# Kernel tuning notes

Measured on AMD Instinct MI355X. Metric: run time of the kernel, lower is better.

## Reference

```python
import jax, jax.numpy as jnp
import numpy as np

C = 1.0          # curvature of PoincareBall
SQRT_C = 1.0
MIN_NORM = 1e-15
PROJ_EPS = 4e-3  # float32 boundary eps used by PoincareBall.proj
N_NODES = 50000


def _norm(x):
    return jnp.clip(jnp.linalg.norm(x, axis=-1, keepdims=True), MIN_NORM)


def _artanh(x):
    return jnp.arctanh(jnp.clip(x, -1.0 + 1e-7, 1.0 - 1e-7))


def proj(x):
    # clip points to the open ball of radius (1-eps)/sqrt(c)
    norm = _norm(x)
    maxnorm = (1.0 - PROJ_EPS) / SQRT_C
    return jnp.where(norm > maxnorm, x / norm * maxnorm, x)


def expmap0(u):
    u_norm = _norm(u)
    return jnp.tanh(SQRT_C * u_norm) * u / (SQRT_C * u_norm)


def logmap0(p):
    p_norm = _norm(p)
    return _artanh(SQRT_C * p_norm) * p / (SQRT_C * p_norm)


def mobius_add(x, y):
    x2 = jnp.sum(x * x, -1, keepdims=True)
    y2 = jnp.sum(y * y, -1, keepdims=True)
    xy = jnp.sum(x * y, -1, keepdims=True)
    num = (1.0 + 2.0 * C * xy + C * y2) * x + (1.0 - C * x2) * y
    den = 1.0 + 2.0 * C * xy + C * C * x2 * y2
    return num / jnp.clip(den, MIN_NORM)


def mobius_matvec(m, x):
    x_norm = _norm(x)
    mx = x @ m.T  # [N, d_out]
    mx_norm = _norm(mx)
    res = jnp.tanh(mx_norm / x_norm * _artanh(SQRT_C * x_norm)) * mx / (mx_norm * SQRT_C)
    zero_row = jnp.all(mx == 0, axis=-1, keepdims=True)
    return jnp.where(zero_row, jnp.zeros_like(res), res)


def setup_inputs() -> dict:
    key = jax.random.key(0)
    k = jax.random.split(key, 6)
    n, d_in, d_out, n_edges = N_NODES, 256, 96, 800000
    # points on the Poincare ball
    x = proj(0.02 * jax.random.normal(k[0], (n, d_in), jnp.float32))
    weight = jax.random.normal(k[1], (d_out, d_in), jnp.float32) * (1.0 / np.sqrt(d_in)).astype(np.float32)
    bias = jax.random.normal(k[2], (d_out,), jnp.float32) * 0.01
    edge_row = jax.random.randint(k[3], (n_edges,), 0, n)
    edge_col = jax.random.randint(k[4], (n_edges,), 0, n)
    # normalized adjacency weights ~ 1/avg_degree
    edge_weight = jax.random.uniform(k[5], (n_edges,), jnp.float32) * (1.0 / 16.0)
    return {"x": x, "weight": weight, "bias": bias, "edge_weight": edge_weight,
            "edge_row": edge_row, "edge_col": edge_col}


def reference(x, weight, bias, edge_weight, edge_row, edge_col):
    # --- HypLinear (dropout inactive in eval) ---
    h = proj(mobius_matvec(weight, x))
    hyp_bias = proj(expmap0(bias[None, :]))  # proj_tan0 is identity on the ball
    h = proj(mobius_add(h, hyp_bias))
    # --- HypAgg: spmm(adj, logmap0(h)) then expmap0 ---
    xt = logmap0(h)                                  # [N, d_out]
    msgs = edge_weight[:, None] * xt[edge_col]       # [E, d_out]
    support = jax.ops.segment_sum(msgs, edge_row, num_segments=N_NODES)
    h = proj(expmap0(support))
    # --- HypAct: relu in tangent space, map back (c_in == c_out) ---
    h = proj(expmap0(jax.nn.relu(logmap0(h))))
    return h
```

## Files before the change

### kernel.cpp

```cpp
#include <hip/hip_runtime.h>


typedef __attribute__((ext_vector_type(8))) short short8;
typedef __attribute__((ext_vector_type(4))) float floatx4;

#define DIN 256
#define DOUT 96
#define MAXN 0.996f
#define EPS15 1e-15f
#define ATC (1.0f - 1e-7f)
#define NBK 391
#define CAP 2560
#define TILE 6144

__device__ __forceinline__ float us2f(unsigned short u) {
    unsigned int v = ((unsigned int)u) << 16;
    return __uint_as_float(v);
}
__device__ __forceinline__ unsigned short f2us(float f) {
    unsigned int b = __float_as_uint(f);
    unsigned int r = (b + 0x7FFFu + ((b >> 16) & 1u)) >> 16;
    return (unsigned short)r;
}

__global__ void initzero_kernel(const unsigned short* __restrict__ xraw,
                                const void* __restrict__ bias,
                                const void* __restrict__ wgt,
                                float* __restrict__ ws,
                                int* __restrict__ gcur) {
    int i = blockIdx.x * blockDim.x + threadIdx.x;
    int stride = gridDim.x * blockDim.x;
    for (int k = i; k < NBK * 16; k += stride) gcur[k] = 0;

    if (blockIdx.x == 0 && threadIdx.x < 64) {
        int l = threadIdx.x;
        float v0 = us2f(xraw[l]);
        float v1 = us2f(xraw[64 + l]);
        int big = (!(fabsf(v0) < 1e4f)) || (!(fabsf(v1) < 1e4f));
        #pragma unroll
        for (int m = 32; m >= 1; m >>= 1) big |= __shfl_xor(big, m, 64);
        bool isb = !big;
        if (l == 0) ws[97] = isb ? 1.0f : 0.0f;

        float b0 = isb ? us2f(((const unsigned short*)bias)[l])
                       : ((const float*)bias)[l];
        float b1 = 0.0f;
        if (l < 32)
            b1 = isb ? us2f(((const unsigned short*)bias)[64 + l])
                     : ((const float*)bias)[64 + l];
        float n2 = b0 * b0 + b1 * b1;
        #pragma unroll
        for (int m = 32; m >= 1; m >>= 1) n2 += __shfl_xor(n2, m, 64);
        float bn = fmaxf(sqrtf(n2), EPS15);
        float ef = tanhf(bn) / bn;
        float hn = ef * sqrtf(n2);
        float s = (hn > MAXN) ? MAXN / fmaxf(hn, EPS15) : 1.0f;
        ws[l] = s * ef * b0;
        if (l < 32) ws[64 + l] = s * ef * b1;
        if (l == 0) { float v = s * hn; ws[96] = v * v; }
    }

    if (blockIdx.x >= 1 && blockIdx.x <= 12) {
        int t = threadIdx.x, lane = t & 63;
        float v0 = us2f(xraw[lane]);
        float v1 = us2f(xraw[64 + lane]);
        int big = (!(fabsf(v0) < 1e4f)) || (!(fabsf(v1) < 1e4f));
        #pragma unroll
        for (int m = 32; m >= 1; m >>= 1) big |= __shfl_xor(big, m, 64);
        bool isb = !big;
        uint4* wz = (uint4*)(ws + 128);
        int g = t + 256 * (int)(blockIdx.x - 1);
        int c = g >> 5, j = g & 31;
        int f = c >> 4, mr = c & 15;
        int kt = j >> 2, q = j & 3;
        if (isb) {
            const uint4* wg = (const uint4*)wgt;
            wz[(f * 8 + kt) * 64 + q * 16 + mr] = wg[g];
        } else {
            const float* wgf = (const float*)wgt;
            const float* src = wgf + (size_t)c * DIN + j * 8;
            unsigned short tmp[8];
            #pragma unroll
            for (int z = 0; z < 8; z++) tmp[z] = f2us(src[z]);
            wz[(f * 8 + kt) * 64 + q * 16 + mr] = *(const uint4*)tmp;
        }
    }
}

__global__ void __launch_bounds__(256) part_kernel(
        const void* __restrict__ ew,
        const int* __restrict__ erow,
        const int* __restrict__ ecol,
        const float* __restrict__ ws,
        int* __restrict__ gcur,
        uint2* __restrict__ arena, int E) {
    __shared__ uint2 stage[TILE];
    __shared__ int h[NBK], excl[NBK], cur[NBK], gb[NBK];
    __shared__ int cb[64];

    const int t = threadIdx.x;
    const bool isb = ws[97] != 0.0f;
    const int tb = blockIdx.x * TILE;
    const int tcnt = min(TILE, E - tb);

    for (int i = t; i < NBK; i += 256) h[i] = 0;
    __syncthreads();

    int rw[24]; unsigned int pk[24];
    #pragma unroll
    for (int k = 0; k < 24; k++) {
        int e = tb + t + 256 * k;
        if (e < E) {
            int r = erow[e];
            unsigned int wb = isb ? (unsigned int)((const unsigned short*)ew)[e]
                                  : (unsigned int)f2us(((const float*)ew)[e]);
            rw[k] = r;
            pk[k] = (wb << 16) | (unsigned int)ecol[e];
            atomicAdd(&h[r >> 7], 1);
        } else rw[k] = -1;
    }
    __syncthreads();

    if (t < 64) {
        int s = 0;
        #pragma unroll
        for (int j = 0; j < 8; j++) {
            int b2 = t * 8 + j;
            if (b2 < NBK) s += h[b2];
        }
        int sc = s;
        #pragma unroll
        for (int d = 1; d < 64; d <<= 1) {
            int tt = __shfl_up(sc, d, 64);
            if (t >= d) sc += tt;
        }
        cb[t] = sc - s;
    }
    __syncthreads();
    for (int b2 = t; b2 < NBK; b2 += 256) {
        int base = cb[b2 >> 3];
        int x = 0;
        for (int j = (b2 & ~7); j < b2; j++) x += h[j];
        excl[b2] = base + x;
        cur[b2]  = base + x;
        gb[b2] = atomicAdd(&gcur[b2 * 16], h[b2]);
    }
    __syncthreads();

    #pragma unroll
    for (int k = 0; k < 24; k++) {
        if (rw[k] >= 0) {
            int b2 = rw[k] >> 7;
            int slot = atomicAdd(&cur[b2], 1);
            stage[slot] = make_uint2(pk[k], (unsigned int)rw[k]);
        }
    }
    __syncthreads();

    for (int s = t; s < tcnt; s += 256) {
        uint2 ent = stage[s];
        int b2 = (int)ent.y >> 7;
        int p = gb[b2] + (s - excl[b2]);
        if (p < CAP) arena[(size_t)b2 * CAP + p] = ent;
    }
}

__global__ void __launch_bounds__(256) hypsort_kernel(
        const void* __restrict__ x,
        float* __restrict__ ws,
        unsigned short* __restrict__ xtb,
        const int* __restrict__ gcur,
        uint2* __restrict__ arena,
        uint2* __restrict__ roff,
        int N) {
    __shared__ int h[128], excl[128], cur[128];

    const int t = threadIdx.x;
    const bool isb = ws[97] != 0.0f;
    const int b = blockIdx.x;
    const int rem = b % 3;
    const int b3 = b / 3;

    if (rem == 2) {
        const int idx = b3;
        int cnt = gcur[idx * 16]; if (cnt > CAP) cnt = CAP;
        const size_t ab = (size_t)idx * CAP;

        for (int i = t; i < 128; i += 256) h[i] = 0;
        __syncthreads();

        uint2 ent[10];
        #pragma unroll
        for (int k = 0; k < 10; k++) {
            int j = t + 256 * k;
            if (j < cnt) {
                ent[k] = arena[ab + j];
                atomicAdd(&h[ent[k].y & 127u], 1);
            } else ent[k] = make_uint2(0u, 0u);
        }
        __syncthreads();

        if (t < 64) {
            int a0 = h[2 * t], a1 = h[2 * t + 1];
            int ps = a0 + a1;
            int sc = ps;
            #pragma unroll
            for (int d = 1; d < 64; d <<= 1) {
                int tt = __shfl_up(sc, d, 64);
                if (t >= d) sc += tt;
            }
            int ex = sc - ps;
            excl[2 * t] = ex;      excl[2 * t + 1] = ex + a0;
            cur[2 * t]  = ex;      cur[2 * t + 1]  = ex + a0;
        }
        __syncthreads();

        if (t < 128)
            roff[idx * 128 + t] =
                make_uint2((unsigned int)(ab + excl[t]), (unsigned int)h[t]);
        #pragma unroll
        for (int k = 0; k < 10; k++) {
            int j = t + 256 * k;
            if (j < cnt) {
                int slot = atomicAdd(&cur[ent[k].y & 127u], 1);
                arena[ab + slot] = ent[k];
            }
        }
        return;
    }

    const int idx = b3 * 2 + rem;
    const int lane = t & 63;
    const int wv = t >> 6;
    const int mrow = lane & 15;
    const int quad = lane >> 4;
    const uint4* __restrict__ Wg = (const uint4*)(ws + 128);

    const int r0 = (idx * 4 + wv) * 16;
    if (r0 >= N) return;

    float hbl[6];
    #pragma unroll
    for (int f = 0; f < 6; f++) hbl[f] = ws[mrow + 16 * f];
    const float hb2 = ws[96];

    int xr = r0 + mrow; if (xr >= N) xr = N - 1;
    short8 afrag[8];
    if (isb) {
        const unsigned short* xrow = (const unsigned short*)x + (size_t)xr * DIN + quad * 8;
        #pragma unroll
        for (int kt = 0; kt < 8; kt++)
            afrag[kt] = *(const short8*)(xrow + kt * 32);
    } else {
        const float* xrow = (const float*)x + (size_t)xr * DIN + quad * 8;
        #pragma unroll
        for (int kt = 0; kt < 8; kt++) {
            short8 a;
            #pragma unroll
            for (int j = 0; j < 8; j++) a[j] = (short)f2us(xrow[kt * 32 + j]);
            afrag[kt] = a;
        }
    }

    float xn2p = 0.f;
    #pragma unroll
    for (int kt = 0; kt < 8; kt++)
        #pragma unroll
        for (int j = 0; j < 8; j++) {
            float v = us2f((unsigned short)afrag[kt][j]);
            xn2p = fmaf(v, v, xn2p);
        }
    xn2p += __shfl_xor(xn2p, 16, 64);
    xn2p += __shfl_xor(xn2p, 32, 64);

    floatx4 acc[6];
    #pragma unroll
    for (int f = 0; f < 6; f++) acc[f] = (floatx4){0.f, 0.f, 0.f, 0.f};
    #pragma unroll
    for (int f = 0; f < 6; f++) {
        uint4 bw[8];
        #pragma unroll
        for (int kt = 0; kt < 8; kt++)
            bw[kt] = Wg[(f * 8 + kt) * 64 + lane];
        #pragma unroll
        for (int kt = 0; kt < 8; kt++) {
            short8 bfr = *(const short8*)&bw[kt];
            acc[f] = __builtin_amdgcn_mfma_f32_16x16x32_bf16(afrag[kt], bfr, acc[f], 0, 0, 0);
        }
    }

    float mxn2[4], dmh[4];
    #pragma unroll
    for (int reg = 0; reg < 4; reg++) {
        float a2 = 0.f, ad = 0.f;
        #pragma unroll
        for (int f = 0; f < 6; f++) {
            float v = acc[f][reg];
            a2 = fmaf(v, v, a2);
            ad = fmaf(v, hbl[f], ad);
        }
        mxn2[reg] = a2; dmh[reg] = ad;
    }
    #pragma unroll
    for (int m = 8; m >= 1; m >>= 1)
        #pragma unroll
        for (int reg = 0; reg < 4; reg++) {
            mxn2[reg] += __shfl_xor(mxn2[reg], m, 64);
            dmh[reg]  += __shfl_xor(dmh[reg],  m, 64);
        }

    int sel = mrow & 3;
    float xn2  = __shfl(xn2p, quad * 4 + sel, 64);
    float wmx2 = mxn2[sel], wdmh = dmh[sel];

    float xn  = fmaxf(sqrtf(xn2), EPS15);
    float mxn = fmaxf(sqrtf(wmx2), EPS15);
    float g   = (mxn / xn) * atanhf(fminf(xn, ATC));
    float tg  = tanhf(g);
    float rs0 = tg / mxn;
    float rn  = rs0 * sqrtf(wmx2);
    float s1  = (rn > MAXN) ? MAXN / fmaxf(rn, EPS15) : 1.0f;
    float al  = s1 * rs0;
    float x2  = al * al * wmx2;
    float xy  = al * wdmh;
    float cA  = 1.0f + 2.0f * xy + hb2;
    float cB  = 1.0f - x2;
    float den = fmaxf(1.0f + 2.0f * xy + x2 * hb2, EPS15);
    float p   = cA * al / den;
    float qq  = cB / den;
    float o2  = p*p*wmx2 + 2.0f*p*qq*wdmh + qq*qq*hb2;
    float on  = sqrtf(fmaxf(o2, 0.0f));
    float s2  = (on > MAXN) ? MAXN / fmaxf(on, EPS15) : 1.0f;
    float pn  = fmaxf(s2 * on, EPS15);
    float F   = (atanhf(fminf(pn, ATC)) / pn) * s2;
    float Fp_m = F * p, Fq_m = F * qq;

    float Fp[4], Fq[4];
    #pragma unroll
    for (int reg = 0; reg < 4; reg++) {
        Fp[reg] = __shfl(Fp_m, quad * 16 + reg, 64);
        Fq[reg] = __shfl(Fq_m, quad * 16 + reg, 64);
    }

    #pragma unroll
    for (int reg = 0; reg < 4; reg++) {
        int row = r0 + quad * 4 + reg;
        if (row < N) {
            size_t base = (size_t)row * DOUT + mrow;
            #pragma unroll
            for (int f = 0; f < 6; f++)
                xtb[base + 16 * f] = f2us(fmaf(Fp[reg], acc[f][reg], Fq[reg] * hbl[f]));
        }
    }
}

__global__ void __launch_bounds__(256) rowagg_kernel(
        const unsigned short* __restrict__ xtb,
        const uint2* __restrict__ arena,
        const uint2* __restrict__ roff,
        const float* __restrict__ ws,
        void* __restrict__ out, int N) {
    int wv = threadIdx.x >> 6, lane = threadIdx.x & 63;
    int node = blockIdx.x * 4 + wv;
    if (node >= N) return;
    const bool isb = ws[97] != 0.0f;
    const bool act = lane < 48;

    uint2 ro = roff[node];
    unsigned int start = ro.x;
    int cnt = (int)ro.y;

    float acc0 = 0.f, acc1 = 0.f;

    unsigned int uA[8], uB[8];
    float wA[8], wB[8];

#define ISSUE(BU, BW, B)                                                       \
    _Pragma("unroll")                                                          \
    for (int k = 0; k < 8; k++) {                                              \
        int idx = (B) * 8 + k;                                                 \
        unsigned int ex = (unsigned int)__shfl((int)myx, idx, 64);             \
        BW[k] = __uint_as_float(ex & 0xFFFF0000u);                             \
        const unsigned int* sp =                                               \
            (const unsigned int*)(xtb + (size_t)(ex & 0xFFFFu) * DOUT);        \
        BU[k] = (act && idx < navail) ? sp[lane] : 0u;                         \
    }

#define CONSUME(BU, BW)                                                        \
    _Pragma("unroll")                                                          \
    for (int k = 0; k < 8; k++) {                                              \
        acc0 = fmaf(BW[k], __uint_as_float(BU[k] << 16), acc0);                \
        acc1 = fmaf(BW[k], __uint_as_float(BU[k] & 0xFFFF0000u), acc1);        \
    }

    for (int cs = 0; cs < cnt; cs += 64) {
        int navail = cnt - cs; if (navail > 64) navail = 64;
        unsigned int myx = (lane < navail) ? arena[start + cs + lane].x : 0u;
        int nb = (navail + 7) >> 3;
        ISSUE(uA, wA, 0);
        for (int bb = 1; bb < nb; bb++) {
            if (bb & 1) { ISSUE(uB, wB, bb); CONSUME(uA, wA); }
            else        { ISSUE(uA, wA, bb); CONSUME(uB, wB); }
        }
        if (nb & 1) { CONSUME(uA, wA); }
        else        { CONSUME(uB, wB); }
    }
#undef ISSUE
#undef CONSUME

    float u0 = acc0, u1 = acc1;
    float n2 = u0*u0 + u1*u1;
    #pragma unroll
    for (int m = 32; m >= 1; m >>= 1) n2 += __shfl_xor(n2, m, 64);
    float un = fmaxf(sqrtf(n2), EPS15);
    float ef = tanhf(un) / un;
    float p0 = ef * u0, p1 = ef * u1;
    float pnrm = ef * sqrtf(n2);
    float sc = (pnrm > MAXN) ? MAXN / fmaxf(pnrm, EPS15) : 1.0f;
    p0 *= sc; p1 *= sc; pnrm *= sc;
    float pncl = fmaxf(pnrm, EPS15);
    float lf = atanhf(fminf(pncl, ATC)) / pncl;
    float t0 = fmaxf(lf * p0, 0.0f), t1 = fmaxf(lf * p1, 0.0f);
    float tn2 = t0*t0 + t1*t1;
    #pragma unroll
    for (int m = 32; m >= 1; m >>= 1) tn2 += __shfl_xor(tn2, m, 64);
    float tn = fmaxf(sqrtf(tn2), EPS15);
    float ef2 = tanhf(tn) / tn;
    float en = ef2 * sqrtf(tn2);
    float s2 = (en > MAXN) ? MAXN / fmaxf(en, EPS15) : 1.0f;
    float scale = s2 * ef2;
    float v0 = scale * t0, v1 = scale * t1;

    if (act) {
        if (isb) {
            unsigned int pk = ((unsigned int)f2us(v1) << 16) | (unsigned int)f2us(v0);
            ((unsigned int*)((unsigned short*)out + (size_t)node * DOUT))[lane] = pk;
        } else {
            float2 fv; fv.x = v0; fv.y = v1;
            ((float2*)((float*)out + (size_t)node * DOUT))[lane] = fv;
        }
    }
}

extern "C" void kernel_launch(void* const* d_in, const int* in_sizes, int n_in,
                              void* d_out, int out_size, void* d_ws, size_t ws_size,
                              hipStream_t stream) {
    const void* x    = d_in[0];
    const void* wgt  = d_in[1];
    const void* bias = d_in[2];
    const void* ew   = d_in[3];
    const int* erow  = (const int*)d_in[4];
    const int* ecol  = (const int*)d_in[5];

    int N = out_size / DOUT;
    int E = in_sizes[4];

    float* wsf = (float*)d_ws;
    int* gcur = (int*)(wsf + 128 + 12288);
    uint2* arena = (uint2*)((char*)d_ws + 74688);
    unsigned short* xtb = (unsigned short*)((char*)d_ws + 74688 + (size_t)NBK * CAP * 8);
    uint2* roff = (uint2*)(xtb + (size_t)N * DOUT);

    int Pb = (E + TILE - 1) / TILE;

    initzero_kernel<<<13, 256, 0, stream>>>((const unsigned short*)x, bias, wgt, wsf, gcur);
    part_kernel<<<Pb, 256, 0, stream>>>(ew, erow, ecol, wsf, gcur, arena, E);
    hypsort_kernel<<<3 * NBK, 256, 0, stream>>>(x, wsf, xtb, gcur, arena, roff, N);
    rowagg_kernel<<<(N + 3) / 4, 256, 0, stream>>>(xtb, arena, roff, wsf, d_out, N);
}
```

Measured before the change: 184.8 us.

## Split fused hyp/sort kernel, pad per-row edge lists to multiples of eight

Splits the combined matvec and bucket-sort kernel into separate hyp and sort kernels. The sort stage now pads each row's edge list to a multiple of 8 with zero entries and stores a precomputed byte offset plus the weight bits, so the aggregation loop can drop its bounds checks and per-edge index multiply. The partition tile size is halved and the bucket capacity raised, giving more part blocks with fewer registers each. The cost is an extra kernel launch, padding writes, and wasted loads on zero-weight padded entries.

```diff
diff --git a/kernel.cpp b/kernel.cpp
--- a/kernel.cpp
+++ b/kernel.cpp
@@ -10,8 +10,8 @@
 #define EPS15 1e-15f
 #define ATC (1.0f - 1e-7f)
 #define NBK 391
-#define CAP 2560
-#define TILE 6144
+#define CAP 3072
+#define TILE 3072
 
 __device__ __forceinline__ float us2f(unsigned short u) {
     unsigned int v = ((unsigned int)u) << 16;
@@ -106,9 +106,9 @@
     for (int i = t; i < NBK; i += 256) h[i] = 0;
     __syncthreads();
 
-    int rw[24]; unsigned int pk[24];
-    #pragma unroll
-    for (int k = 0; k < 24; k++) {
+    int rw[12]; unsigned int pk[12];
+    #pragma unroll
+    for (int k = 0; k < 12; k++) {
         int e = tb + t + 256 * k;
         if (e < E) {
             int r = erow[e];
@@ -148,7 +148,7 @@
     __syncthreads();
 
     #pragma unroll
-    for (int k = 0; k < 24; k++) {
+    for (int k = 0; k < 12; k++) {
         if (rw[k] >= 0) {
             int b2 = rw[k] >> 7;
             int slot = atomicAdd(&cur[b2], 1);
@@ -165,78 +165,19 @@
     }
 }
 
-__global__ void __launch_bounds__(256) hypsort_kernel(
-        const void* __restrict__ x,
-        float* __restrict__ ws,
-        unsigned short* __restrict__ xtb,
-        const int* __restrict__ gcur,
-        uint2* __restrict__ arena,
-        uint2* __restrict__ roff,
-        int N) {
-    __shared__ int h[128], excl[128], cur[128];
-
+__global__ void hyp_kernel(const void* __restrict__ x,
+                           float* __restrict__ ws,
+                           unsigned short* __restrict__ xtb,
+                           int N) {
     const int t = threadIdx.x;
     const bool isb = ws[97] != 0.0f;
-    const int b = blockIdx.x;
-    const int rem = b % 3;
-    const int b3 = b / 3;
-
-    if (rem == 2) {
-        const int idx = b3;
-        int cnt = gcur[idx * 16]; if (cnt > CAP) cnt = CAP;
-        const size_t ab = (size_t)idx * CAP;
-
-        for (int i = t; i < 128; i += 256) h[i] = 0;
-        __syncthreads();
-
-        uint2 ent[10];
-        #pragma unroll
-        for (int k = 0; k < 10; k++) {
-            int j = t + 256 * k;
-            if (j < cnt) {
-                ent[k] = arena[ab + j];
-                atomicAdd(&h[ent[k].y & 127u], 1);
-            } else ent[k] = make_uint2(0u, 0u);
-        }
-        __syncthreads();
-
-        if (t < 64) {
-            int a0 = h[2 * t], a1 = h[2 * t + 1];
-            int ps = a0 + a1;
-            int sc = ps;
-            #pragma unroll
-            for (int d = 1; d < 64; d <<= 1) {
-                int tt = __shfl_up(sc, d, 64);
-                if (t >= d) sc += tt;
-            }
-            int ex = sc - ps;
-            excl[2 * t] = ex;      excl[2 * t + 1] = ex + a0;
-            cur[2 * t]  = ex;      cur[2 * t + 1]  = ex + a0;
-        }
-        __syncthreads();
-
-        if (t < 128)
-            roff[idx * 128 + t] =
-                make_uint2((unsigned int)(ab + excl[t]), (unsigned int)h[t]);
-        #pragma unroll
-        for (int k = 0; k < 10; k++) {
-            int j = t + 256 * k;
-            if (j < cnt) {
-                int slot = atomicAdd(&cur[ent[k].y & 127u], 1);
-                arena[ab + slot] = ent[k];
-            }
-        }
-        return;
-    }
-
-    const int idx = b3 * 2 + rem;
     const int lane = t & 63;
     const int wv = t >> 6;
     const int mrow = lane & 15;
     const int quad = lane >> 4;
     const uint4* __restrict__ Wg = (const uint4*)(ws + 128);
 
-    const int r0 = (idx * 4 + wv) * 16;
+    const int r0 = ((int)blockIdx.x * 4 + wv) * 16;
     if (r0 >= N) return;
 
     float hbl[6];
@@ -354,6 +295,72 @@
     }
 }
 
+__global__ void __launch_bounds__(256) sortg_kernel(
+        const int* __restrict__ gcur,
+        uint2* __restrict__ arena,
+        uint2* __restrict__ roff) {
+    __shared__ int h[128], h8[128], excl[128], cur[128];
+
+    const int t = threadIdx.x;
+    const int idx = blockIdx.x;
+    int cnt = gcur[idx * 16]; if (cnt > CAP) cnt = CAP;
+    const size_t ab = (size_t)idx * CAP;
+
+    for (int i = t; i < 128; i += 256) h[i] = 0;
+    __syncthreads();
+
+    uint2 ent[12];
+    #pragma unroll
+    for (int k = 0; k < 12; k++) {
+        int j = t + 256 * k;
+        if (j < cnt) {
+            ent[k] = arena[ab + j];
+            atomicAdd(&h[ent[k].y & 127u], 1);
+        } else ent[k] = make_uint2(0u, 0u);
+    }
+    __syncthreads();
+
+    if (t < 64) {
+        int a0 = h[2 * t], a1 = h[2 * t + 1];
+        int p0 = (a0 + 7) & ~7, p1 = (a1 + 7) & ~7;
+        int ps = p0 + p1;
+        int sc = ps;
+        #pragma unroll
+        for (int d = 1; d < 64; d <<= 1) {
+            int tt = __shfl_up(sc, d, 64);
+            if (t >= d) sc += tt;
+        }
+        int ex = sc - ps;
+        h8[2 * t] = p0;        h8[2 * t + 1] = p1;
+        excl[2 * t] = ex;      excl[2 * t + 1] = ex + p0;
+        cur[2 * t]  = ex;      cur[2 * t + 1]  = ex + p0;
+    }
+    __syncthreads();
+
+    if (t < 128) {
+        int e8 = excl[t];
+        int c8 = h8[t];
+        if (e8 > CAP) e8 = CAP;
+        if (e8 + c8 > CAP) c8 = CAP - e8;
+        if (c8 < 0) c8 = 0;
+        roff[idx * 128 + t] =
+            make_uint2((unsigned int)(ab + e8), (unsigned int)c8);
+        for (int j = excl[t] + h[t]; j < excl[t] + h8[t]; j++)
+            if (j < CAP) arena[ab + j] = make_uint2(0u, 0u);
+    }
+    #pragma unroll
+    for (int k = 0; k < 12; k++) {
+        int j = t + 256 * k;
+        if (j < cnt) {
+            int slot = atomicAdd(&cur[ent[k].y & 127u], 1);
+            if (slot < CAP)
+                arena[ab + slot] =
+                    make_uint2((ent[k].x & 0xFFFFu) * 192u,
+                               ent[k].x & 0xFFFF0000u);
+        }
+    }
+}
+
 __global__ void __launch_bounds__(256) rowagg_kernel(
         const unsigned short* __restrict__ xtb,
         const uint2* __restrict__ arena,
@@ -368,10 +375,12 @@
 
     uint2 ro = roff[node];
     unsigned int start = ro.x;
-    int cnt = (int)ro.y;
+    int cnt8 = (int)ro.y;
+
+    const char* __restrict__ xc = (const char*)xtb;
+    const unsigned int lane4 = (unsigned int)lane * 4u;
 
     float acc0 = 0.f, acc1 = 0.f;
-
     unsigned int uA[8], uB[8];
     float wA[8], wB[8];
 
@@ -379,11 +388,9 @@
     _Pragma("unroll")                                                          \
     for (int k = 0; k < 8; k++) {                                              \
         int idx = (B) * 8 + k;                                                 \
-        unsigned int ex = (unsigned int)__shfl((int)myx, idx, 64);             \
-        BW[k] = __uint_as_float(ex & 0xFFFF0000u);                             \
-        const unsigned int* sp =                                               \
-            (const unsigned int*)(xtb + (size_t)(ex & 0xFFFFu) * DOUT);        \
-        BU[k] = (act && idx < navail) ? sp[lane] : 0u;                         \
+        unsigned int off = (unsigned int)__shfl((int)my.x, idx, 64);           \
+        BW[k] = __uint_as_float((unsigned int)__shfl((int)my.y, idx, 64));     \
+        BU[k] = *(const unsigned int*)(xc + off + lane4);                      \
     }
 
 #define CONSUME(BU, BW)                                                        \
@@ -393,10 +400,10 @@
         acc1 = fmaf(BW[k], __uint_as_float(BU[k] & 0xFFFF0000u), acc1);        \
     }
 
-    for (int cs = 0; cs < cnt; cs += 64) {
-        int navail = cnt - cs; if (navail > 64) navail = 64;
-        unsigned int myx = (lane < navail) ? arena[start + cs + lane].x : 0u;
-        int nb = (navail + 7) >> 3;
+    for (int cs = 0; cs < cnt8; cs += 64) {
+        int navail = cnt8 - cs; if (navail > 64) navail = 64;
+        uint2 my = arena[start + cs + lane];
+        int nb = navail >> 3;
         ISSUE(uA, wA, 0);
         for (int bb = 1; bb < nb; bb++) {
             if (bb & 1) { ISSUE(uB, wB, bb); CONSUME(uA, wA); }
@@ -407,6 +414,8 @@
     }
 #undef ISSUE
 #undef CONSUME
+
+    if (!act) { acc0 = 0.f; acc1 = 0.f; }
 
     float u0 = acc0, u1 = acc1;
     float n2 = u0*u0 + u1*u1;
@@ -462,9 +471,11 @@
     uint2* roff = (uint2*)(xtb + (size_t)N * DOUT);
 
     int Pb = (E + TILE - 1) / TILE;
+    int Hb = (N + 63) / 64;
 
     initzero_kernel<<<13, 256, 0, stream>>>((const unsigned short*)x, bias, wgt, wsf, gcur);
     part_kernel<<<Pb, 256, 0, stream>>>(ew, erow, ecol, wsf, gcur, arena, E);
-    hypsort_kernel<<<3 * NBK, 256, 0, stream>>>(x, wsf, xtb, gcur, arena, roff, N);
+    hyp_kernel<<<Hb, 256, 0, stream>>>(x, wsf, xtb, N);
+    sortg_kernel<<<NBK, 256, 0, stream>>>(gcur, arena, roff);
     rowagg_kernel<<<(N + 3) / 4, 256, 0, stream>>>(xtb, arena, roff, wsf, d_out, N);
 }
```

New measurement: 184.2 us. No clear change (-0.3%).
